# Performance work log

Hardware: AMD Instinct MI355X
Metric: run time of the kernel (lower is better)

Reference implementation:

```python
import jax, jax.numpy as jnp
import numpy as np

NUM_HEADS = 16
LN_EPS = 1e-5


def setup_inputs() -> dict:
    key = jax.random.key(0)
    ks = jax.random.split(key, 6)
    B, N, D = 4, 4096, 1024
    s = 1.0 / np.sqrt(D)
    return {
        "x": jax.random.normal(ks[0], (B, N, D), dtype=jnp.float32),
        "Wq": jax.random.normal(ks[1], (D, D), dtype=jnp.float32) * s,
        "Wk": jax.random.normal(ks[2], (D, D), dtype=jnp.float32) * s,
        "Wv": jax.random.normal(ks[3], (D, D), dtype=jnp.float32) * s,
        "Wo": jax.random.normal(ks[4], (D, D), dtype=jnp.float32) * s,
        "bo": jnp.zeros((D,), dtype=jnp.float32),
        "alpha": jax.random.uniform(ks[5], (1,), dtype=jnp.float32),
        "temperature": jnp.float32(1.0),
        "gamma": jnp.ones((D,), dtype=jnp.float32),
        "beta": jnp.zeros((D,), dtype=jnp.float32),
    }


def _layernorm(x, gamma, beta):
    mu = jnp.mean(x, axis=-1, keepdims=True)
    var = jnp.var(x, axis=-1, keepdims=True)
    return (x - mu) * jax.lax.rsqrt(var + LN_EPS) * gamma + beta


def reference(x, Wq, Wk, Wv, Wo, bo, alpha, temperature, gamma, beta):
    B, N, D = x.shape
    H = NUM_HEADS
    hd = D // H
    residual = x
    # projections (query=None -> query comes from x), nn.Linear: x @ W.T
    q = (x @ Wq.T).reshape(B, N, H, hd).transpose(0, 2, 1, 3)  # [B,H,N,hd]
    k = (x @ Wk.T).reshape(B, N, H, hd).transpose(0, 2, 1, 3)
    v = (x @ Wv.T).reshape(B, N, H, hd).transpose(0, 2, 1, 3)
    # kk = K^T K + alpha*I, per (batch, head): [B,H,hd,hd]
    kk = jnp.einsum('bhnd,bhne->bhde', k, k)
    kk = kk + alpha[0] * jnp.eye(hd, dtype=x.dtype)
    kk_inv = jnp.linalg.inv(kk)
    # attn_map = kk_inv @ K^T @ V : [B,H,hd,hd]
    ktv = jnp.einsum('bhnd,bhne->bhde', k, v)
    attn_map = kk_inv @ ktv
    attn_map = jax.nn.softmax(attn_map / temperature, axis=-2)
    out = q @ attn_map  # [B,H,N,hd]
    out = out.transpose(0, 2, 1, 3).reshape(B, N, D)
    out = out @ Wo.T + bo
    return _layernorm(out + residual, gamma, beta)
```

## Files before the change

kernel.cpp:

```cpp
#include <hip/hip_runtime.h>
#include <cstdint>
#include <cstddef>

typedef unsigned short u16;
typedef __bf16 bf16x8 __attribute__((ext_vector_type(8)));
typedef float f32x4 __attribute__((ext_vector_type(4)));
typedef u16 u16x8 __attribute__((ext_vector_type(8)));
typedef u16 u16x4 __attribute__((ext_vector_type(4)));

#define NB 4
#define NN 4096
#define ND 1024
#define NH 16
#define NTOK (NB * NN)

__device__ __forceinline__ u16 f2bf(float f) {
    unsigned u = __float_as_uint(f);
    u += 0x7fffu + ((u >> 16) & 1u);
    return (u16)(u >> 16);
}

__device__ __forceinline__ void gload_lds16(const void* g, void* l) {
    __builtin_amdgcn_global_load_lds(
        (const __attribute__((address_space(1))) void*)g,
        (__attribute__((address_space(3))) void*)l, 16, 0, 0);
}

__global__ __launch_bounds__(256) void prep_cast(
    const float* __restrict__ x,
    const float* __restrict__ wq, const float* __restrict__ wk,
    const float* __restrict__ wv, const float* __restrict__ wo,
    u16* __restrict__ xb, u16* __restrict__ wb)
{
    const int n_x4 = (NTOK * ND) / 4;
    const int n_w4 = (ND * ND) / 4;
    const int total = n_x4 + 4 * n_w4;
    for (int i = blockIdx.x * blockDim.x + threadIdx.x; i < total;
         i += gridDim.x * blockDim.x) {
        float4 v;
        u16* dst;
        if (i < n_x4) {
            v = ((const float4*)x)[i];
            dst = xb + (size_t)i * 4;
        } else {
            int j = i - n_x4;
            int w = j / n_w4;
            int off = j - w * n_w4;
            const float* src = (w == 0) ? wq : (w == 1) ? wk : (w == 2) ? wv : wo;
            v = ((const float4*)src)[off];
            dst = wb + (size_t)j * 4;
        }
        u16x4 o;
        o[0] = f2bf(v.x); o[1] = f2bf(v.y); o[2] = f2bf(v.z); o[3] = f2bf(v.w);
        *(u16x4*)dst = o;
    }
}

template <int OUT_MODE>
__global__ __launch_bounds__(256, 2) void gemm_bt(
    const u16* __restrict__ A, int lda,
    const u16* __restrict__ Bw, int ldb,
    void* __restrict__ Cout, int ldc, int K,
    const float* __restrict__ bias, const float* __restrict__ resid,
    int rows_per_batch, size_t b_stride)
{
    __shared__ alignas(16) u16 lA[128 * 32];
    __shared__ alignas(16) u16 lB[128 * 32];

    const int tid = threadIdx.x;
    const int wv = tid >> 6, lane = tid & 63;
    const int quad = lane >> 4, lrow = lane & 15;
    const int row0 = blockIdx.y * 128, col0 = blockIdx.x * 128;
    const int wm = (wv >> 1) * 64, wn = (wv & 1) * 64;

    const u16* Bp = Bw + (b_stride ? (size_t)(row0 / rows_per_batch) * b_stride : 0);

    f32x4 acc[4][4] = {};

    const int srow = lane >> 2;
    const int scolh = (lane & 3) * 8;

    for (int k0 = 0; k0 < K; k0 += 32) {
        __syncthreads();
        const int c0 = wv * 2;
#pragma unroll
        for (int c = c0; c < c0 + 2; ++c) {
            int row = c * 16 + srow;
            gload_lds16(A + (size_t)(row0 + row) * lda + k0 + scolh, &lA[c * 512]);
            gload_lds16(Bp + (size_t)(col0 + row) * ldb + k0 + scolh, &lB[c * 512]);
        }
        __syncthreads();

        bf16x8 af[4], bfv[4];
#pragma unroll
        for (int t = 0; t < 4; ++t)
            af[t] = *(const bf16x8*)&lA[(wm + t * 16 + lrow) * 32 + quad * 8];
#pragma unroll
        for (int t = 0; t < 4; ++t)
            bfv[t] = *(const bf16x8*)&lB[(wn + t * 16 + lrow) * 32 + quad * 8];

#pragma unroll
        for (int mt = 0; mt < 4; ++mt)
#pragma unroll
            for (int nt = 0; nt < 4; ++nt)
                acc[mt][nt] = __builtin_amdgcn_mfma_f32_16x16x32_bf16(
                    af[mt], bfv[nt], acc[mt][nt], 0, 0, 0);
    }

#pragma unroll
    for (int mt = 0; mt < 4; ++mt)
#pragma unroll
        for (int nt = 0; nt < 4; ++nt)
#pragma unroll
            for (int r = 0; r < 4; ++r) {
                int grow = row0 + wm + mt * 16 + quad * 4 + r;
                int gcol = col0 + wn + nt * 16 + lrow;
                if (OUT_MODE == 0) {
                    ((u16*)Cout)[(size_t)grow * ldc + gcol] = f2bf(acc[mt][nt][r]);
                } else {
                    float vv = acc[mt][nt][r] + bias[gcol] +
                               resid[(size_t)grow * ldc + gcol];
                    ((float*)Cout)[(size_t)grow * ldc + gcol] = vv;
                }
            }
}

__global__ __launch_bounds__(256) void stage2a_kernel(
    const u16* __restrict__ qkv,
    float* __restrict__ Part)
{
    __shared__ alignas(16) u16 sKt[4][64][40];
    __shared__ alignas(16) u16 sVt[4][64][40];
    __shared__ float S[64][132];

    const int tid = threadIdx.x;
    const int wv = tid >> 6, lane = tid & 63;
    const int quad = lane >> 4, lrow = lane & 15;
    const int bh = blockIdx.x, split = blockIdx.y;
    const int b = bh >> 4, h = bh & 15;

    f32x4 akk[4][4] = {};
    f32x4 aktv[4][4] = {};
    const u16* kbase = qkv + ND + h * 64;
    const u16* vbase = qkv + 2 * ND + h * 64;
    const size_t tok0 = (size_t)b * NN;

    for (int it = 0; it < 2; ++it) {
        const int n0 = split * 256 + wv * 64 + it * 32;
#pragma unroll
        for (int pass = 0; pass < 4; ++pass) {
            int nl = pass * 8 + (lane >> 3);
            int d0 = (lane & 7) * 8;
            size_t roff = (tok0 + n0 + nl) * 3072 + d0;
            u16x8 kvv = *(const u16x8*)(kbase + roff);
            u16x8 vvv = *(const u16x8*)(vbase + roff);
#pragma unroll
            for (int j = 0; j < 8; ++j) {
                sKt[wv][d0 + j][nl] = kvv[j];
                sVt[wv][d0 + j][nl] = vvv[j];
            }
        }
        bf16x8 fK[4], fV[4];
#pragma unroll
        for (int t = 0; t < 4; ++t) {
            fK[t] = *(const bf16x8*)&sKt[wv][t * 16 + lrow][quad * 8];
            fV[t] = *(const bf16x8*)&sVt[wv][t * 16 + lrow][quad * 8];
        }
#pragma unroll
        for (int mt = 0; mt < 4; ++mt)
#pragma unroll
            for (int et = 0; et < 4; ++et) {
                akk[mt][et] = __builtin_amdgcn_mfma_f32_16x16x32_bf16(
                    fK[mt], fK[et], akk[mt][et], 0, 0, 0);
                aktv[mt][et] = __builtin_amdgcn_mfma_f32_16x16x32_bf16(
                    fK[mt], fV[et], aktv[mt][et], 0, 0, 0);
            }
    }

    for (int w = 0; w < 4; ++w) {
        if (wv == w) {
#pragma unroll
            for (int mt = 0; mt < 4; ++mt)
#pragma unroll
                for (int et = 0; et < 4; ++et)
#pragma unroll
                    for (int r = 0; r < 4; ++r) {
                        int row = mt * 16 + quad * 4 + r;
                        int col = et * 16 + lrow;
                        if (w == 0) {
                            S[row][col] = akk[mt][et][r];
                            S[row][64 + col] = aktv[mt][et][r];
                        } else {
                            S[row][col] += akk[mt][et][r];
                            S[row][64 + col] += aktv[mt][et][r];
                        }
                    }
        }
        __syncthreads();
    }

    float* dst = Part + (size_t)(bh * 16 + split) * 8192;
#pragma unroll
    for (int c = 0; c < 8; ++c) {
        int idx = tid * 4 + c * 1024;
        int row = idx >> 7, col = idx & 127;
        float4 v = *(const float4*)&S[row][col];
        ((float4*)dst)[idx >> 2] = v;
    }
}

__global__ __launch_bounds__(256) void stage2b_kernel(
    const float* __restrict__ Part,
    const u16* __restrict__ wb,
    const float* __restrict__ alpha,
    const float* __restrict__ temp,
    u16* __restrict__ Mout)
{
    __shared__ float S[64][132];
    __shared__ float colbuf[2][64];
    __shared__ alignas(16) u16 sAttn[64][72];

    const int tid = threadIdx.x;
    const int wv = tid >> 6, lane = tid & 63;
    const int quad = lane >> 4, lrow = lane & 15;
    const int b = blockIdx.x >> 4, h = blockIdx.x & 15;

    const float* Pb = Part + (size_t)blockIdx.x * 16 * 8192;
#pragma unroll
    for (int c = 0; c < 8; ++c) {
        int idx = tid * 4 + c * 1024;
        float4 a = ((const float4*)Pb)[idx >> 2];
#pragma unroll
        for (int s = 1; s < 16; ++s) {
            float4 t4 = ((const float4*)(Pb + (size_t)s * 8192))[idx >> 2];
            a.x += t4.x; a.y += t4.y; a.z += t4.z; a.w += t4.w;
        }
        int row = idx >> 7, col = idx & 127;
        *(float4*)&S[row][col] = a;
    }
    __syncthreads();

    const float aval = alpha[0];
    const int c0 = wv * 32;
    float R[32];
#pragma unroll
    for (int j = 0; j < 32; ++j) {
        R[j] = S[lane][c0 + j];
        if (c0 + j == lane) R[j] += aval;
    }
    if (wv == 0) colbuf[0][lane] = R[0];
    __syncthreads();

    float mydiag = 1.0f;
    for (int p = 0; p < 64; ++p) {
        const int cur = p & 1;
        float cv = colbuf[cur][lane];
        float pv = colbuf[cur][p];
        if (p == lane) mydiag = pv;
        float m = (lane == p) ? 0.0f : cv * __builtin_amdgcn_rcpf(pv);
#pragma unroll
        for (int j = 0; j < 32; ++j) {
            float rowv = __uint_as_float(
                __builtin_amdgcn_readlane(__float_as_uint(R[j]), p));
            R[j] -= m * rowv;
        }
        if (p < 63) {
            int pn = p + 1;
            if (wv == (pn >> 5)) colbuf[cur ^ 1][lane] = R[pn & 31];
        }
        __syncthreads();
    }

    if (wv >= 2) {
        const float idg = __builtin_amdgcn_rcpf(mydiag) * (1.0f / temp[0]);
#pragma unroll
        for (int j = 0; j < 32; ++j) {
            float xv = R[j] * idg;
            float mx = xv;
#pragma unroll
            for (int off = 32; off > 0; off >>= 1)
                mx = fmaxf(mx, __shfl_xor(mx, off, 64));
            float ev = __expf(xv - mx);
            float sum = ev;
#pragma unroll
            for (int off = 32; off > 0; off >>= 1)
                sum += __shfl_xor(sum, off, 64);
            sAttn[lane][(wv - 2) * 32 + j] = f2bf(ev * __builtin_amdgcn_rcpf(sum));
        }
    }
    __syncthreads();

    {
        bf16x8 fB[4][2];
#pragma unroll
        for (int nt = 0; nt < 4; ++nt)
#pragma unroll
            for (int ks = 0; ks < 2; ++ks)
                fB[nt][ks] = *(const bf16x8*)&sAttn[nt * 16 + lrow][ks * 32 + quad * 8];

        const u16* wo = wb + (size_t)3072 * ND + h * 64;
        u16* Mb = Mout + (size_t)b * ND * ND + h * 64;
        for (int i = 0; i < 16; ++i) {
            int mt = wv * 16 + i;
            int oA = mt * 16 + lrow;
            bf16x8 fA[2];
#pragma unroll
            for (int ks = 0; ks < 2; ++ks)
                fA[ks] = *(const bf16x8*)(wo + (size_t)oA * ND + ks * 32 + quad * 8);
#pragma unroll
            for (int nt = 0; nt < 4; ++nt) {
                f32x4 acc = {};
                acc = __builtin_amdgcn_mfma_f32_16x16x32_bf16(fA[0], fB[nt][0], acc, 0, 0, 0);
                acc = __builtin_amdgcn_mfma_f32_16x16x32_bf16(fA[1], fB[nt][1], acc, 0, 0, 0);
#pragma unroll
                for (int r = 0; r < 4; ++r) {
                    int o = mt * 16 + quad * 4 + r;
                    Mb[(size_t)o * ND + nt * 16 + lrow] = f2bf(acc[r]);
                }
            }
        }
    }
}

__global__ __launch_bounds__(256) void ln_kernel(
    const float* __restrict__ y, const float* __restrict__ gamma,
    const float* __restrict__ beta, float* __restrict__ out)
{
    const int row = blockIdx.x, tid = threadIdx.x;
    const float4 v = ((const float4*)(y + (size_t)row * ND))[tid];
    float s = v.x + v.y + v.z + v.w;
    float q = v.x * v.x + v.y * v.y + v.z * v.z + v.w * v.w;
#pragma unroll
    for (int off = 32; off > 0; off >>= 1) {
        s += __shfl_xor(s, off, 64);
        q += __shfl_xor(q, off, 64);
    }
    __shared__ float ss[4], sq[4];
    const int wv = tid >> 6;
    if ((tid & 63) == 0) { ss[wv] = s; sq[wv] = q; }
    __syncthreads();
    s = ss[0] + ss[1] + ss[2] + ss[3];
    q = sq[0] + sq[1] + sq[2] + sq[3];
    const float mu = s * (1.0f / ND);
    const float var = q * (1.0f / ND) - mu * mu;
    const float rs = rsqrtf(var + 1e-5f);
    const float4 g = ((const float4*)gamma)[tid];
    const float4 bt = ((const float4*)beta)[tid];
    float4 o;
    o.x = (v.x - mu) * rs * g.x + bt.x;
    o.y = (v.y - mu) * rs * g.y + bt.y;
    o.z = (v.z - mu) * rs * g.z + bt.z;
    o.w = (v.w - mu) * rs * g.w + bt.w;
    ((float4*)(out + (size_t)row * ND))[tid] = o;
}

extern "C" void kernel_launch(void* const* d_in, const int* in_sizes, int n_in,
                              void* d_out, int out_size, void* d_ws, size_t ws_size,
                              hipStream_t stream)
{
    const float* x     = (const float*)d_in[0];
    const float* Wq    = (const float*)d_in[1];
    const float* Wk    = (const float*)d_in[2];
    const float* Wv    = (const float*)d_in[3];
    const float* Wo    = (const float*)d_in[4];
    const float* bo    = (const float*)d_in[5];
    const float* alpha = (const float*)d_in[6];
    const float* temp  = (const float*)d_in[7];
    const float* gamma = (const float*)d_in[8];
    const float* beta  = (const float*)d_in[9];

    char* ws = (char*)d_ws;
    u16* xb   = (u16*)(ws);
    float* Part = (float*)(ws);
    u16* wb   = (u16*)(ws + 33554432);
    u16* qkv  = (u16*)(ws + 41943040);
    u16* Mb   = (u16*)(ws + 142606336);
    float* y  = (float*)(ws + 150994944);
    float* out = (float*)d_out;

    prep_cast<<<dim3(4096), dim3(256), 0, stream>>>(x, Wq, Wk, Wv, Wo, xb, wb);

    gemm_bt<0><<<dim3(24, 128), dim3(256), 0, stream>>>(
        xb, 1024, wb, 1024, (void*)qkv, 3072, 1024,
        nullptr, nullptr, 1 << 30, (size_t)0);

    stage2a_kernel<<<dim3(64, 16), dim3(256), 0, stream>>>(qkv, Part);
    stage2b_kernel<<<dim3(64), dim3(256), 0, stream>>>(Part, wb, alpha, temp, Mb);

    gemm_bt<1><<<dim3(8, 128), dim3(256), 0, stream>>>(
        qkv, 3072, Mb, 1024, (void*)y, 1024, 1024,
        bo, x, 4096, (size_t)(1024 * 1024));

    ln_kernel<<<dim3(16384), dim3(256), 0, stream>>>(y, gamma, beta, out);
}
```

Baseline: 441.0 us.

## Enlarge GEMM tile to 256x128 with K=64 and XOR-swizzled LDS layout

```diff
diff --git a/kernel.cpp b/kernel.cpp
--- a/kernel.cpp
+++ b/kernel.cpp
@@ -64,51 +64,64 @@
     const float* __restrict__ bias, const float* __restrict__ resid,
     int rows_per_batch, size_t b_stride)
 {
-    __shared__ alignas(16) u16 lA[128 * 32];
-    __shared__ alignas(16) u16 lB[128 * 32];
+    __shared__ alignas(16) u16 lA[256 * 64];
+    __shared__ alignas(16) u16 lB[128 * 64];
 
     const int tid = threadIdx.x;
     const int wv = tid >> 6, lane = tid & 63;
     const int quad = lane >> 4, lrow = lane & 15;
-    const int row0 = blockIdx.y * 128, col0 = blockIdx.x * 128;
-    const int wm = (wv >> 1) * 64, wn = (wv & 1) * 64;
+    const int row0 = blockIdx.y * 256, col0 = blockIdx.x * 128;
+    const int wm = (wv >> 1) * 128, wn = (wv & 1) * 64;
 
     const u16* Bp = Bw + (b_stride ? (size_t)(row0 / rows_per_batch) * b_stride : 0);
 
-    f32x4 acc[4][4] = {};
-
-    const int srow = lane >> 2;
-    const int scolh = (lane & 3) * 8;
-
-    for (int k0 = 0; k0 < K; k0 += 32) {
+    f32x4 acc[8][4] = {};
+
+    const int srow = lane >> 3;
+    const int cswE = ((lane & 7) ^ srow) * 8;
+
+    for (int k0 = 0; k0 < K; k0 += 64) {
         __syncthreads();
-        const int c0 = wv * 2;
-#pragma unroll
-        for (int c = c0; c < c0 + 2; ++c) {
-            int row = c * 16 + srow;
-            gload_lds16(A + (size_t)(row0 + row) * lda + k0 + scolh, &lA[c * 512]);
-            gload_lds16(Bp + (size_t)(col0 + row) * ldb + k0 + scolh, &lB[c * 512]);
+#pragma unroll
+        for (int i = 0; i < 8; ++i) {
+            int rb = wv * 64 + i * 8;
+            gload_lds16(A + (size_t)(row0 + rb + srow) * lda + k0 + cswE,
+                        &lA[rb * 64]);
+        }
+#pragma unroll
+        for (int i = 0; i < 4; ++i) {
+            int rb = wv * 32 + i * 8;
+            gload_lds16(Bp + (size_t)(col0 + rb + srow) * ldb + k0 + cswE,
+                        &lB[rb * 64]);
         }
         __syncthreads();
 
-        bf16x8 af[4], bfv[4];
-#pragma unroll
-        for (int t = 0; t < 4; ++t)
-            af[t] = *(const bf16x8*)&lA[(wm + t * 16 + lrow) * 32 + quad * 8];
-#pragma unroll
-        for (int t = 0; t < 4; ++t)
-            bfv[t] = *(const bf16x8*)&lB[(wn + t * 16 + lrow) * 32 + quad * 8];
-
-#pragma unroll
-        for (int mt = 0; mt < 4; ++mt)
-#pragma unroll
-            for (int nt = 0; nt < 4; ++nt)
-                acc[mt][nt] = __builtin_amdgcn_mfma_f32_16x16x32_bf16(
-                    af[mt], bfv[nt], acc[mt][nt], 0, 0, 0);
-    }
-
-#pragma unroll
-    for (int mt = 0; mt < 4; ++mt)
+#pragma unroll
+        for (int kc = 0; kc < 2; ++kc) {
+            const int ch = ((kc * 4 + quad) ^ (lrow & 7)) * 8;
+            bf16x8 bfv[4];
+#pragma unroll
+            for (int t = 0; t < 4; ++t)
+                bfv[t] = *(const bf16x8*)&lB[(wn + t * 16 + lrow) * 64 + ch];
+#pragma unroll
+            for (int mt = 0; mt < 8; ++mt) {
+                bf16x8 af = *(const bf16x8*)&lA[(wm + mt * 16 + lrow) * 64 + ch];
+#pragma unroll
+                for (int nt = 0; nt < 4; ++nt)
+                    acc[mt][nt] = __builtin_amdgcn_mfma_f32_16x16x32_bf16(
+                        af, bfv[nt], acc[mt][nt], 0, 0, 0);
+            }
+        }
+    }
+
+    float bvals[4];
+    if (OUT_MODE == 1) {
+#pragma unroll
+        for (int nt = 0; nt < 4; ++nt)
+            bvals[nt] = bias[col0 + wn + nt * 16 + lrow];
+    }
+#pragma unroll
+    for (int mt = 0; mt < 8; ++mt)
 #pragma unroll
         for (int nt = 0; nt < 4; ++nt)
 #pragma unroll
@@ -118,7 +131,7 @@
                 if (OUT_MODE == 0) {
                     ((u16*)Cout)[(size_t)grow * ldc + gcol] = f2bf(acc[mt][nt][r]);
                 } else {
-                    float vv = acc[mt][nt][r] + bias[gcol] +
+                    float vv = acc[mt][nt][r] + bvals[nt] +
                                resid[(size_t)grow * ldc + gcol];
                     ((float*)Cout)[(size_t)grow * ldc + gcol] = vv;
                 }
@@ -380,14 +393,14 @@
 
     prep_cast<<<dim3(4096), dim3(256), 0, stream>>>(x, Wq, Wk, Wv, Wo, xb, wb);
 
-    gemm_bt<0><<<dim3(24, 128), dim3(256), 0, stream>>>(
+    gemm_bt<0><<<dim3(24, 64), dim3(256), 0, stream>>>(
         xb, 1024, wb, 1024, (void*)qkv, 3072, 1024,
         nullptr, nullptr, 1 << 30, (size_t)0);
 
     stage2a_kernel<<<dim3(64, 16), dim3(256), 0, stream>>>(qkv, Part);
     stage2b_kernel<<<dim3(64), dim3(256), 0, stream>>>(Part, wb, alpha, temp, Mb);
 
-    gemm_bt<1><<<dim3(8, 128), dim3(256), 0, stream>>>(
+    gemm_bt<1><<<dim3(8, 64), dim3(256), 0, stream>>>(
         qkv, 3072, Mb, 1024, (void*)y, 1024, 1024,
         bo, x, 4096, (size_t)(1024 * 1024));
 
```

New measurement: 424.0 us. -3.8%, faster.
